# Optimization experiments

Measured on AMD Instinct MI355X. Metric: run time of the kernel, lower is better.

## Reference

```python
import jax, jax.numpy as jnp
import numpy as np

N_NODES = 50000
N_EDGES = 800000
N_REL = 8
OUT_CH = 64      # latent dim of z
HID = 128        # hidden_channels
IN_CH = 128      # reconstructed feature dim
NEG_SLOPE = 0.2


def rgat_conv(x, src, dst, edge_type, weight, q, k, bias, num_nodes):
    """PyG RGATConv, heads=1, dim=1, additive-self-attention, across-relation.
    x: [N, in]; weight: [R, in, out]; q,k: [out, 1]; bias: [out]."""
    # per-relation transform of all nodes, then per-edge gather (same math as
    # per-edge bmm with weight[edge_type], avoids [E, in, out] intermediate)
    x_all = jnp.einsum('ni,rio->nro', x, weight)          # [N, R, out]
    x_j = x_all[src, edge_type]                            # [E, out]
    x_i = x_all[dst, edge_type]                            # [E, out]
    alpha = (x_i @ q + x_j @ k)[:, 0]                      # [E]
    alpha = jax.nn.leaky_relu(alpha, NEG_SLOPE)
    # scatter-softmax over destination neighborhoods
    m = jax.ops.segment_max(alpha, dst, num_segments=num_nodes)
    m = jnp.where(jnp.isfinite(m), m, 0.0)                 # empty segments -> 0
    ex = jnp.exp(alpha - m[dst])
    denom = jax.ops.segment_sum(ex, dst, num_segments=num_nodes)
    a = ex / (denom[dst] + 1e-16)                          # [E]
    out = jax.ops.segment_sum(a[:, None] * x_j, dst, num_segments=num_nodes)
    return out + bias


def setup_inputs() -> dict:
    key = jax.random.key(0)
    ks = jax.random.split(key, 12)
    z = jax.random.normal(ks[0], (N_NODES, OUT_CH), dtype=jnp.float32)
    edge_index = jax.random.randint(ks[1], (2, N_EDGES), 0, N_NODES, dtype=jnp.int32)
    edge_type = jax.random.randint(ks[2], (N_EDGES,), 0, N_REL, dtype=jnp.int32)

    def glorot(k_, shape):
        fan = shape[-2] + shape[-1]
        return jax.random.normal(k_, shape, dtype=jnp.float32) * jnp.sqrt(2.0 / fan)

    return {
        'z': z,
        'lin_w': glorot(ks[3], (HID, OUT_CH)),
        'lin_b': jnp.zeros((HID,), dtype=jnp.float32),
        'w1': glorot(ks[4], (N_REL, HID, HID)),
        'q1': glorot(ks[5], (HID, 1)),
        'k1': glorot(ks[6], (HID, 1)),
        'b1': jnp.zeros((HID,), dtype=jnp.float32),
        'w2': glorot(ks[7], (N_REL, HID, IN_CH)),
        'q2': glorot(ks[8], (IN_CH, 1)),
        'k2': glorot(ks[9], (IN_CH, 1)),
        'b2': jnp.zeros((IN_CH,), dtype=jnp.float32),
        'edge_index': edge_index,
        'edge_type': edge_type,
    }


def reference(z, lin_w, lin_b, w1, q1, k1, b1, w2, q2, k2, b2, edge_index, edge_type):
    num_nodes = z.shape[0]
    src, dst = edge_index[0], edge_index[1]
    h = z @ lin_w.T + lin_b                                 # nn.Linear
    h = jax.nn.relu(rgat_conv(h, src, dst, edge_type, w1, q1, k1, b1, num_nodes))
    # dropout is identity in eval mode
    recon_x = rgat_conv(h, src, dst, edge_type, w2, q2, k2, b2, num_nodes)
    return recon_x
```

## Files before the change

kernel.cpp:

```cpp
#include <hip/hip_runtime.h>
#include <hip/hip_bf16.h>
#include <cstdint>
#include <cstddef>

#define N_NODES 50000
#define N_EDGES 800000
#define NSEG    (N_NODES * 8)

using frag_t = __attribute__((ext_vector_type(8))) short;
using f32x4  = __attribute__((ext_vector_type(4))) float;

typedef const __attribute__((address_space(1))) void* gptr_t;
typedef __attribute__((address_space(3))) void* lptr_t;

__device__ __forceinline__ short f2bf(float x) {
    __hip_bfloat16 h = __float2bfloat16(x);
    return *reinterpret_cast<short*>(&h);
}
__device__ __forceinline__ float bf2f(unsigned int u) {
    union { unsigned int i; float f; } v;
    v.i = u << 16;
    return v.f;
}
__device__ __forceinline__ unsigned int packbf2(float lo, float hi) {
    unsigned int a = (unsigned short)f2bf(lo);
    unsigned int b = (unsigned short)f2bf(hi);
    return a | (b << 16);
}


__global__ void hist_kernel(const int* __restrict__ dst, const int* __restrict__ et,
                            int* __restrict__ deg8, int E) {
    int e = blockIdx.x * 256 + threadIdx.x;
    if (e < E) atomicAdd(&deg8[dst[e] * 8 + et[e]], 1);
}

__global__ __launch_bounds__(256) void scan_part(const int* __restrict__ deg8,
                                                 int* __restrict__ part, int M) {
    __shared__ int red[256];
    int t = threadIdx.x;
    int idx = blockIdx.x * 1024 + t * 4;
    int s = 0;
    if (idx + 3 < M) {
        int4 d = *(const int4*)(deg8 + idx);
        s = d.x + d.y + d.z + d.w;
    } else {
        for (int c = 0; c < 4; c++) if (idx + c < M) s += deg8[idx + c];
    }
    red[t] = s;
    __syncthreads();
    #pragma unroll
    for (int off = 128; off; off >>= 1) {
        if (t < off) red[t] += red[t + off];
        __syncthreads();
    }
    if (t == 0) part[blockIdx.x] = red[0];
}

__global__ __launch_bounds__(512) void scan_mid(int* __restrict__ part, int nparts,
                                                int* __restrict__ rowp, int M) {
    __shared__ int buf[512];
    int t = threadIdx.x;
    int own = (t < nparts) ? part[t] : 0;
    buf[t] = own;
    __syncthreads();
    for (int off = 1; off < 512; off <<= 1) {
        int v = buf[t];
        int u = (t >= off) ? buf[t - off] : 0;
        __syncthreads();
        buf[t] = v + u;
        __syncthreads();
    }
    if (t < nparts) part[t] = buf[t] - own;
    if (t == 511) rowp[M] = buf[511];
}

__global__ __launch_bounds__(256) void scan_fix(const int* __restrict__ deg8,
                                                const int* __restrict__ part,
                                                int* __restrict__ rowp,
                                                int* __restrict__ cursor, int M) {
    __shared__ int wsum[4];
    int t = threadIdx.x, lane = t & 63, w = t >> 6;
    int idx = blockIdx.x * 1024 + t * 4;
    int v0 = 0, v1 = 0, v2 = 0, v3 = 0;
    if (idx + 3 < M) {
        int4 d = *(const int4*)(deg8 + idx);
        v0 = d.x; v1 = d.y; v2 = d.z; v3 = d.w;
    } else {
        if (idx     < M) v0 = deg8[idx];
        if (idx + 1 < M) v1 = deg8[idx + 1];
        if (idx + 2 < M) v2 = deg8[idx + 2];
        if (idx + 3 < M) v3 = deg8[idx + 3];
    }
    int tsum = v0 + v1 + v2 + v3;
    int sc = tsum;
    #pragma unroll
    for (int off = 1; off < 64; off <<= 1) {
        int u = __shfl_up(sc, off, 64);
        if (lane >= off) sc += u;
    }
    if (lane == 63) wsum[w] = sc;
    __syncthreads();
    int woff = 0;
    for (int i = 0; i < w; i++) woff += wsum[i];
    int excl = part[blockIdx.x] + woff + sc - tsum;
    if (idx     < M) { rowp[idx]     = excl; cursor[idx]     = excl; } excl += v0;
    if (idx + 1 < M) { rowp[idx + 1] = excl; cursor[idx + 1] = excl; } excl += v1;
    if (idx + 2 < M) { rowp[idx + 2] = excl; cursor[idx + 2] = excl; } excl += v2;
    if (idx + 3 < M) { rowp[idx + 3] = excl; cursor[idx + 3] = excl; }
}

__global__ void fill_kernel(const int* __restrict__ src, const int* __restrict__ dst,
                            const int* __restrict__ et, int* __restrict__ cursor,
                            int* __restrict__ sorted, int E) {
    int e = blockIdx.x * 256 + threadIdx.x;
    if (e < E) {
        int pos = atomicAdd(&cursor[dst[e] * 8 + et[e]], 1);
        sorted[pos] = src[e] | (et[e] << 16);
    }
}


__global__ __launch_bounds__(256) void gemm_lin(const float* __restrict__ A,
                                                const float* __restrict__ B,
                                                const float* __restrict__ bias,
                                                unsigned short* __restrict__ hb, int N) {
    const int Kdim = 64;
    __shared__ float As[32][64];
    __shared__ float Bs[32][128];
    int t = threadIdx.x;
    int n0 = blockIdx.x * 64;
    int rg = t >> 4, cg = t & 15;
    int an = t >> 2, ak = (t & 3) * 8;
    float acc[4][8] = {};

    for (int k0 = 0; k0 < Kdim; k0 += 32) {
        int gn = n0 + an;
        if (gn < N) {
            const float* ap = A + (size_t)gn * Kdim + k0 + ak;
            float4 v0 = *(const float4*)ap;
            float4 v1 = *(const float4*)(ap + 4);
            As[ak + 0][an] = v0.x; As[ak + 1][an] = v0.y;
            As[ak + 2][an] = v0.z; As[ak + 3][an] = v0.w;
            As[ak + 4][an] = v1.x; As[ak + 5][an] = v1.y;
            As[ak + 6][an] = v1.z; As[ak + 7][an] = v1.w;
        } else {
            #pragma unroll
            for (int c = 0; c < 8; c++) As[ak + c][an] = 0.f;
        }
        {
            int o = t >> 1, kh = (t & 1) * 16;
            const float* bp = B + (size_t)o * Kdim + k0 + kh;
            #pragma unroll
            for (int j = 0; j < 4; j++) {
                float4 v = ((const float4*)bp)[j];
                Bs[kh + j * 4 + 0][o] = v.x;
                Bs[kh + j * 4 + 1][o] = v.y;
                Bs[kh + j * 4 + 2][o] = v.z;
                Bs[kh + j * 4 + 3][o] = v.w;
            }
        }
        __syncthreads();
        #pragma unroll
        for (int k = 0; k < 32; k++) {
            float a[4], b[8];
            *(float4*)&a[0] = *(const float4*)&As[k][rg * 4];
            *(float4*)&b[0] = *(const float4*)&Bs[k][cg * 8];
            *(float4*)&b[4] = *(const float4*)&Bs[k][cg * 8 + 4];
            #pragma unroll
            for (int i = 0; i < 4; i++)
                #pragma unroll
                for (int j = 0; j < 8; j++)
                    acc[i][j] = fmaf(a[i], b[j], acc[i][j]);
        }
        __syncthreads();
    }
    #pragma unroll
    for (int i = 0; i < 4; i++) {
        int gn = n0 + rg * 4 + i;
        if (gn < N) {
            unsigned short us[8];
            #pragma unroll
            for (int j = 0; j < 8; j++)
                us[j] = (unsigned short)f2bf(acc[i][j] + bias[cg * 8 + j]);
            *(int4*)(hb + (size_t)gn * 128 + cg * 8) = *(int4*)&us[0];
        }
    }
}


__global__ void wprep_kernel(const float* __restrict__ W, const float* __restrict__ q,
                             const float* __restrict__ k, short* __restrict__ Bf,
                             float* __restrict__ wq, float* __restrict__ wk) {
    int g = blockIdx.x * 256 + threadIdx.x;
    if (g < 131072) {
        int kk = g >> 7, o = g & 127;
        float v = W[(size_t)kk * 128 + o];
        Bf[(((size_t)(kk >> 3) * 128) + o) * 8 + (kk & 7)] = f2bf(v);
        return;
    }
    int h = g - 131072;
    if (h < 2048) {
        int which = h >> 10;
        int r = (h >> 7) & 7;
        int i = h & 127;
        const float* vec = which ? k : q;
        const float* wrow = W + ((size_t)r * 128 + i) * 128;
        float acc = 0.f;
        #pragma unroll 4
        for (int o = 0; o < 128; o++) acc = fmaf(wrow[o], vec[o], acc);
        (which ? wk : wq)[r * 128 + i] = acc;
    }
}


__global__ __launch_bounds__(256) void qk_table_kernel(const unsigned short* __restrict__ xb,
                                                       const float* __restrict__ wq,
                                                       const float* __restrict__ wk,
                                                       float* __restrict__ Q,
                                                       float* __restrict__ K, int N) {
    int n = blockIdx.x * 256 + threadIdx.x;
    if (n >= N) return;
    const uint2* row = (const uint2*)(xb + (size_t)n * 128);
    float aq[8] = {}, ak[8] = {};
    for (int i = 0; i < 32; i++) {
        uint2 d = row[i];
        float x0 = bf2f(d.x & 0xFFFFu);
        float x1 = bf2f(d.x >> 16);
        float x2 = bf2f(d.y & 0xFFFFu);
        float x3 = bf2f(d.y >> 16);
        int c = i * 4;
        #pragma unroll
        for (int r = 0; r < 8; r++) {
            const float* wqr = wq + r * 128 + c;
            const float* wkr = wk + r * 128 + c;
            aq[r] = fmaf(x0, wqr[0], fmaf(x1, wqr[1], fmaf(x2, wqr[2], fmaf(x3, wqr[3], aq[r]))));
            ak[r] = fmaf(x0, wkr[0], fmaf(x1, wkr[1], fmaf(x2, wkr[2], fmaf(x3, wkr[3], ak[r]))));
        }
    }
    float4* qp = (float4*)(Q + (size_t)n * 8);
    qp[0] = *(float4*)&aq[0];
    qp[1] = *(float4*)&aq[4];
    float4* kp = (float4*)(K + (size_t)n * 8);
    kp[0] = *(float4*)&ak[0];
    kp[1] = *(float4*)&ak[4];
}


__global__ __launch_bounds__(512, 8) void fused_agg_gemm(
        const unsigned short* __restrict__ hb,
        const float* __restrict__ Q,
        const float* __restrict__ Kt,
        const int* __restrict__ rowp8,
        const int* __restrict__ sorted,
        const short* __restrict__ Bf,
        const float* __restrict__ bias,
        float* __restrict__ Cout,
        unsigned short* __restrict__ hbout,
        int N, int relu) {
    __shared__ short s_tile[16 * 1024];
    unsigned int* sdw = (unsigned int*)s_tile;
    const unsigned int* hbu = (const unsigned int*)hb;

    int t = threadIdx.x;
    int w = t >> 6, lane = t & 63;
    int lhi = lane >> 4, llo = lane & 15;
    int n0 = blockIdx.x * 16;

    for (int nd = 0; nd < 2; nd++) {
        int row = w * 2 + nd;
        int n = n0 + row;
        float2 acc = {0.f, 0.f};
        int rcur = 0;
        auto flushw = [&](unsigned int val) {
            int kb = rcur * 16 + (lane >> 2);
            sdw[kb * 64 + ((row ^ (kb & 15)) * 4) + (lane & 3)] = val;
        };
        if (n >= N) {
            while (rcur < 8) { flushw(0u); rcur++; }
            continue;
        }
        int beg = rowp8[n * 8];
        int end = rowp8[n * 8 + 8];
        int deg = end - beg;
        if (deg == 0) {
            while (rcur < 8) { flushw(0u); rcur++; }
            continue;
        }

        if (deg <= 64) {
            int pk = 0;
            float a = -INFINITY;
            if (lane < deg) {
                pk = sorted[beg + lane];
                int srcn = pk & 0xFFFF, etj = pk >> 16;
                a = Q[(size_t)n * 8 + etj] + Kt[(size_t)srcn * 8 + etj];
                a = (a > 0.f) ? a : 0.2f * a;
            }
            float m = a;
            #pragma unroll
            for (int off = 32; off; off >>= 1) m = fmaxf(m, __shfl_xor(m, off, 64));
            float e = (lane < deg) ? __expf(a - m) : 0.f;
            float sum = e;
            #pragma unroll
            for (int off = 32; off; off >>= 1) sum += __shfl_xor(sum, off, 64);
            float wgt = e / (sum + 1e-16f);

            int j = 0;
            for (; j + 8 <= deg; j += 8) {
                int pp[8]; float ww[8]; unsigned int dd[8];
                #pragma unroll
                for (int i = 0; i < 8; i++) {
                    pp[i] = __shfl(pk, j + i, 64);
                    ww[i] = __shfl(wgt, j + i, 64);
                }
                #pragma unroll
                for (int i = 0; i < 8; i++)
                    dd[i] = hbu[(size_t)(pp[i] & 0xFFFF) * 64 + lane];
                #pragma unroll
                for (int i = 0; i < 8; i++) {
                    int e0 = pp[i] >> 16;
                    while (rcur < e0) { flushw(packbf2(acc.x, acc.y)); acc.x = acc.y = 0.f; rcur++; }
                    acc.x = fmaf(ww[i], bf2f(dd[i] & 0xFFFF), acc.x);
                    acc.y = fmaf(ww[i], bf2f(dd[i] >> 16),    acc.y);
                }
            }
            for (; j < deg; j++) {
                int   p0 = __shfl(pk, j, 64);
                float w0 = __shfl(wgt, j, 64);
                unsigned int d0 = hbu[(size_t)(p0 & 0xFFFF) * 64 + lane];
                int e0 = p0 >> 16;
                while (rcur < e0) { flushw(packbf2(acc.x, acc.y)); acc.x = acc.y = 0.f; rcur++; }
                acc.x = fmaf(w0, bf2f(d0 & 0xFFFF), acc.x);
                acc.y = fmaf(w0, bf2f(d0 >> 16),    acc.y);
            }
            while (rcur < 8) { flushw(packbf2(acc.x, acc.y)); acc.x = acc.y = 0.f; rcur++; }
        } else {
            auto logit = [&](int j) -> float {
                int pk2 = sorted[beg + j];
                int srcn = pk2 & 0xFFFF, etj = pk2 >> 16;
                float aa = Q[(size_t)n * 8 + etj] + Kt[(size_t)srcn * 8 + etj];
                return (aa > 0.f) ? aa : 0.2f * aa;
            };
            float m = -INFINITY;
            for (int j = lane; j < deg; j += 64) m = fmaxf(m, logit(j));
            #pragma unroll
            for (int off = 32; off; off >>= 1) m = fmaxf(m, __shfl_xor(m, off, 64));
            float sum = 0.f;
            for (int j = lane; j < deg; j += 64) sum += __expf(logit(j) - m);
            #pragma unroll
            for (int off = 32; off; off >>= 1) sum += __shfl_xor(sum, off, 64);
            float inv = 1.f / (sum + 1e-16f);

            for (int j0 = 0; j0 < deg; j0 += 64) {
                int cnt = min(64, deg - j0);
                int pk = 0;
                float wgt = 0.f;
                if (lane < cnt) {
                    pk = sorted[beg + j0 + lane];
                    int srcn = pk & 0xFFFF, etj = pk >> 16;
                    float aa = Q[(size_t)n * 8 + etj] + Kt[(size_t)srcn * 8 + etj];
                    aa = (aa > 0.f) ? aa : 0.2f * aa;
                    wgt = __expf(aa - m) * inv;
                }
                for (int j = 0; j < cnt; j++) {
                    int   p0 = __shfl(pk, j, 64);
                    float w0 = __shfl(wgt, j, 64);
                    unsigned int d0 = hbu[(size_t)(p0 & 0xFFFF) * 64 + lane];
                    int e0 = p0 >> 16;
                    while (rcur < e0) { flushw(packbf2(acc.x, acc.y)); acc.x = acc.y = 0.f; rcur++; }
                    acc.x = fmaf(w0, bf2f(d0 & 0xFFFF), acc.x);
                    acc.y = fmaf(w0, bf2f(d0 >> 16),    acc.y);
                }
            }
            while (rcur < 8) { flushw(packbf2(acc.x, acc.y)); acc.x = acc.y = 0.f; rcur++; }
        }
    }
    __syncthreads();

    int ctb = w;
    f32x4 acc0 = {};
    const char* BfB = (const char*)Bf;
    #pragma unroll 4
    for (int kq = 0; kq < 32; kq++) {
        int kb = kq * 4 + lhi;
        int d = kb * 64 + ((llo ^ (kb & 15)) * 4);
        frag_t a  = *(const frag_t*)(&sdw[d]);
        frag_t b0 = *(const frag_t*)(BfB + ((size_t)kb * 128 + ctb * 16 + llo) * 16);
        acc0 = __builtin_amdgcn_mfma_f32_16x16x32_bf16(a, b0, acc0, 0, 0, 0);
    }

    {
        int col = ctb * 16 + llo;
        float bv = bias[col];
        #pragma unroll
        for (int rg = 0; rg < 4; rg++) {
            int rown = n0 + lhi * 4 + rg;
            if (rown < N) {
                float v = acc0[rg] + bv;
                if (relu) v = fmaxf(v, 0.f);
                if (Cout)  Cout[(size_t)rown * 128 + col] = v;
                if (hbout) hbout[(size_t)rown * 128 + col] = (unsigned short)f2bf(v);
            }
        }
    }
}


extern "C" void kernel_launch(void* const* d_in, const int* in_sizes, int n_in,
                              void* d_out, int out_size, void* d_ws, size_t ws_size,
                              hipStream_t stream) {
    const float* z     = (const float*)d_in[0];
    const float* lin_w = (const float*)d_in[1];
    const float* lin_b = (const float*)d_in[2];
    const float* w1    = (const float*)d_in[3];
    const float* q1    = (const float*)d_in[4];
    const float* k1    = (const float*)d_in[5];
    const float* b1    = (const float*)d_in[6];
    const float* w2    = (const float*)d_in[7];
    const float* q2    = (const float*)d_in[8];
    const float* k2    = (const float*)d_in[9];
    const float* b2    = (const float*)d_in[10];
    const int*   ei    = (const int*)d_in[11];
    const int*   et    = (const int*)d_in[12];
    float* out = (float*)d_out;

    char* ws = (char*)d_ws;
    size_t off = 0;
    auto alloc = [&](size_t bytes) -> void* {
        void* p = ws + off;
        off += (bytes + 255) & ~(size_t)255;
        return p;
    };
    unsigned short* hb  = (unsigned short*)alloc((size_t)N_NODES * 128 * 2);
    unsigned short* hb2 = (unsigned short*)alloc((size_t)N_NODES * 128 * 2);
    float* Q     = (float*)alloc((size_t)N_NODES * 8 * 4);
    float* K     = (float*)alloc((size_t)N_NODES * 8 * 4);
    int* sorted  = (int*)alloc((size_t)N_EDGES * 4);
    int* deg8    = (int*)alloc((size_t)NSEG * 4);
    int* rowp8   = (int*)alloc((size_t)(NSEG + 1) * 4);
    int* cursor8 = (int*)alloc((size_t)NSEG * 4);
    int* part    = (int*)alloc(1024 * 4);
    float* wq    = (float*)alloc(8 * 128 * 4);
    float* wk    = (float*)alloc(8 * 128 * 4);
    short* Bf    = (short*)alloc((size_t)1024 * 128 * 2);

    const int* src = ei;
    const int* dst = ei + N_EDGES;

    const int M = NSEG;
    const int nparts = (M + 1023) / 1024;

    hipMemsetAsync(deg8, 0, (size_t)M * 4, stream);
    hist_kernel<<<(N_EDGES + 255) / 256, 256, 0, stream>>>(dst, et, deg8, N_EDGES);
    scan_part<<<nparts, 256, 0, stream>>>(deg8, part, M);
    scan_mid<<<1, 512, 0, stream>>>(part, nparts, rowp8, M);
    scan_fix<<<nparts, 256, 0, stream>>>(deg8, part, rowp8, cursor8, M);
    fill_kernel<<<(N_EDGES + 255) / 256, 256, 0, stream>>>(src, dst, et, cursor8, sorted, N_EDGES);

    gemm_lin<<<(N_NODES + 63) / 64, 256, 0, stream>>>(z, lin_w, lin_b, hb, N_NODES);

    int fgrid = (N_NODES + 15) / 16;
    int qgrid = (N_NODES + 255) / 256;
    int wgrid = (131072 + 2048) / 256;

    wprep_kernel<<<wgrid, 256, 0, stream>>>(w1, q1, k1, Bf, wq, wk);
    qk_table_kernel<<<qgrid, 256, 0, stream>>>(hb, wq, wk, Q, K, N_NODES);
    fused_agg_gemm<<<fgrid, 512, 0, stream>>>(hb, Q, K, rowp8, sorted, Bf, b1,
                                              (float*)nullptr, hb2, N_NODES, 1);

    wprep_kernel<<<wgrid, 256, 0, stream>>>(w2, q2, k2, Bf, wq, wk);
    qk_table_kernel<<<qgrid, 256, 0, stream>>>(hb2, wq, wk, Q, K, N_NODES);
    fused_agg_gemm<<<fgrid, 512, 0, stream>>>(hb2, Q, K, rowp8, sorted, Bf, b2,
                                              out, (unsigned short*)nullptr, N_NODES, 0);
}
```

Baseline: 375.1 us.

## Process nodes in descending-degree order via counting-sort permutation in fused aggregation

Builds a permutation of nodes sorted by in-degree (descending, capped at 255) using a histogram, a single-block scan and an atomic fill. The fused aggregate+GEMM kernel then processes nodes in that order, so each 16-node tile holds nodes of similar degree and heavy tiles start first. It writes outputs through the permuted node ids. The aim is less load imbalance and wave divergence inside blocks, at the cost of extra setup kernels and scattered output rows and inputs.

Result: slower. 626.3 us (+67.0%).

```diff
diff --git a/kernel.cpp b/kernel.cpp
--- a/kernel.cpp
+++ b/kernel.cpp
@@ -112,11 +112,42 @@
 
 __global__ void fill_kernel(const int* __restrict__ src, const int* __restrict__ dst,
                             const int* __restrict__ et, int* __restrict__ cursor,
-                            int* __restrict__ sorted, int E) {
+                            int* __restrict__ sorted, int E,
+                            const int* __restrict__ rowp8, int* __restrict__ dcount, int N) {
     int e = blockIdx.x * 256 + threadIdx.x;
     if (e < E) {
         int pos = atomicAdd(&cursor[dst[e] * 8 + et[e]], 1);
         sorted[pos] = src[e] | (et[e] << 16);
+    }
+    if (e < N) {
+        int d = min(rowp8[e * 8 + 8] - rowp8[e * 8], 255);
+        atomicAdd(&dcount[255 - d], 1);
+    }
+}
+
+__global__ __launch_bounds__(256) void deg_scan_kernel(const int* __restrict__ dcount,
+                                                       int* __restrict__ dcursor) {
+    __shared__ int buf[256];
+    int t = threadIdx.x;
+    int v = dcount[t];
+    buf[t] = v;
+    __syncthreads();
+    for (int off = 1; off < 256; off <<= 1) {
+        int u = (t >= off) ? buf[t - off] : 0;
+        __syncthreads();
+        buf[t] += u;
+        __syncthreads();
+    }
+    dcursor[t] = buf[t] - v;
+}
+
+__global__ void deg_fill_kernel(const int* __restrict__ rowp8, int* __restrict__ dcursor,
+                                int* __restrict__ perm, int N) {
+    int n = blockIdx.x * 256 + threadIdx.x;
+    if (n < N) {
+        int d = min(rowp8[n * 8 + 8] - rowp8[n * 8], 255);
+        int pos = atomicAdd(&dcursor[255 - d], 1);
+        perm[pos] = n;
     }
 }
 
@@ -253,12 +284,14 @@
         const float* __restrict__ Kt,
         const int* __restrict__ rowp8,
         const int* __restrict__ sorted,
+        const int* __restrict__ perm,
         const short* __restrict__ Bf,
         const float* __restrict__ bias,
         float* __restrict__ Cout,
         unsigned short* __restrict__ hbout,
         int N, int relu) {
     __shared__ short s_tile[16 * 1024];
+    __shared__ int nid_tile[16];
     unsigned int* sdw = (unsigned int*)s_tile;
     const unsigned int* hbu = (const unsigned int*)hb;
 
@@ -269,14 +302,16 @@
 
     for (int nd = 0; nd < 2; nd++) {
         int row = w * 2 + nd;
-        int n = n0 + row;
+        int vrow = n0 + row;
+        int n = (vrow < N) ? perm[vrow] : -1;
+        if (lane == 0) nid_tile[row] = n;
         float2 acc = {0.f, 0.f};
         int rcur = 0;
         auto flushw = [&](unsigned int val) {
             int kb = rcur * 16 + (lane >> 2);
             sdw[kb * 64 + ((row ^ (kb & 15)) * 4) + (lane & 3)] = val;
         };
-        if (n >= N) {
+        if (n < 0) {
             while (rcur < 8) { flushw(0u); rcur++; }
             continue;
         }
@@ -395,12 +430,12 @@
         float bv = bias[col];
         #pragma unroll
         for (int rg = 0; rg < 4; rg++) {
-            int rown = n0 + lhi * 4 + rg;
-            if (rown < N) {
+            int nid = nid_tile[lhi * 4 + rg];
+            if (nid >= 0) {
                 float v = acc0[rg] + bv;
                 if (relu) v = fmaxf(v, 0.f);
-                if (Cout)  Cout[(size_t)rown * 128 + col] = v;
-                if (hbout) hbout[(size_t)rown * 128 + col] = (unsigned short)f2bf(v);
+                if (Cout)  Cout[(size_t)nid * 128 + col] = v;
+                if (hbout) hbout[(size_t)nid * 128 + col] = (unsigned short)f2bf(v);
             }
         }
     }
@@ -441,6 +476,9 @@
     int* rowp8   = (int*)alloc((size_t)(NSEG + 1) * 4);
     int* cursor8 = (int*)alloc((size_t)NSEG * 4);
     int* part    = (int*)alloc(1024 * 4);
+    int* perm    = (int*)alloc((size_t)N_NODES * 4);
+    int* dcount  = (int*)alloc(256 * 4);
+    int* dcursor = (int*)alloc(256 * 4);
     float* wq    = (float*)alloc(8 * 128 * 4);
     float* wk    = (float*)alloc(8 * 128 * 4);
     short* Bf    = (short*)alloc((size_t)1024 * 128 * 2);
@@ -452,11 +490,15 @@
     const int nparts = (M + 1023) / 1024;
 
     hipMemsetAsync(deg8, 0, (size_t)M * 4, stream);
+    hipMemsetAsync(dcount, 0, 256 * 4, stream);
     hist_kernel<<<(N_EDGES + 255) / 256, 256, 0, stream>>>(dst, et, deg8, N_EDGES);
     scan_part<<<nparts, 256, 0, stream>>>(deg8, part, M);
     scan_mid<<<1, 512, 0, stream>>>(part, nparts, rowp8, M);
     scan_fix<<<nparts, 256, 0, stream>>>(deg8, part, rowp8, cursor8, M);
-    fill_kernel<<<(N_EDGES + 255) / 256, 256, 0, stream>>>(src, dst, et, cursor8, sorted, N_EDGES);
+    fill_kernel<<<(N_EDGES + 255) / 256, 256, 0, stream>>>(src, dst, et, cursor8, sorted,
+                                                           N_EDGES, rowp8, dcount, N_NODES);
+    deg_scan_kernel<<<1, 256, 0, stream>>>(dcount, dcursor);
+    deg_fill_kernel<<<(N_NODES + 255) / 256, 256, 0, stream>>>(rowp8, dcursor, perm, N_NODES);
 
     gemm_lin<<<(N_NODES + 63) / 64, 256, 0, stream>>>(z, lin_w, lin_b, hb, N_NODES);
 
@@ -466,11 +508,11 @@
 
     wprep_kernel<<<wgrid, 256, 0, stream>>>(w1, q1, k1, Bf, wq, wk);
     qk_table_kernel<<<qgrid, 256, 0, stream>>>(hb, wq, wk, Q, K, N_NODES);
-    fused_agg_gemm<<<fgrid, 512, 0, stream>>>(hb, Q, K, rowp8, sorted, Bf, b1,
+    fused_agg_gemm<<<fgrid, 512, 0, stream>>>(hb, Q, K, rowp8, sorted, perm, Bf, b1,
                                               (float*)nullptr, hb2, N_NODES, 1);
 
     wprep_kernel<<<wgrid, 256, 0, stream>>>(w2, q2, k2, Bf, wq, wk);
     qk_table_kernel<<<qgrid, 256, 0, stream>>>(hb2, wq, wk, Q, K, N_NODES);
-    fused_agg_gemm<<<fgrid, 512, 0, stream>>>(hb2, Q, K, rowp8, sorted, Bf, b2,
+    fused_agg_gemm<<<fgrid, 512, 0, stream>>>(hb2, Q, K, rowp8, sorted, perm, Bf, b2,
                                               out, (unsigned short*)nullptr, N_NODES, 0);
 }
```

## Dynamically assign rows to waves and broadcast edge data via LDS stash

Applied to the files above, without the earlier changes.

Replaces the fixed two-rows-per-wave assignment with an LDS atomic counter, so waves pull destination rows dynamically and degree imbalance is evened out within a block. Per-edge packed index and softmax weight are stored once into a per-wave LDS stash and read back as broadcast loads, instead of two cross-lane shuffles per edge. This adds an atomic per row, an extra barrier and some extra LDS usage, which may reduce occupancy slightly.

After: 377.1 us. Within noise of the previous version (+0.5%).

```diff
diff --git a/kernel.cpp b/kernel.cpp
--- a/kernel.cpp
+++ b/kernel.cpp
@@ -259,6 +259,8 @@
         unsigned short* __restrict__ hbout,
         int N, int relu) {
     __shared__ short s_tile[16 * 1024];
+    __shared__ uint2 stash[8][64];
+    __shared__ int wcnt;
     unsigned int* sdw = (unsigned int*)s_tile;
     const unsigned int* hbu = (const unsigned int*)hb;
 
@@ -267,8 +269,14 @@
     int lhi = lane >> 4, llo = lane & 15;
     int n0 = blockIdx.x * 16;
 
-    for (int nd = 0; nd < 2; nd++) {
-        int row = w * 2 + nd;
+    if (t == 0) wcnt = 0;
+    __syncthreads();
+
+    for (;;) {
+        int row;
+        if (lane == 0) row = atomicAdd(&wcnt, 1);
+        row = __shfl(row, 0, 64);
+        if (row >= 16) break;
         int n = n0 + row;
         float2 acc = {0.f, 0.f};
         int rcur = 0;
@@ -305,31 +313,30 @@
             #pragma unroll
             for (int off = 32; off; off >>= 1) sum += __shfl_xor(sum, off, 64);
             float wgt = e / (sum + 1e-16f);
+            stash[w][lane] = make_uint2((unsigned int)pk, __float_as_uint(wgt));
 
             int j = 0;
             for (; j + 8 <= deg; j += 8) {
-                int pp[8]; float ww[8]; unsigned int dd[8];
+                uint2 ee[8]; unsigned int dd[8];
+                #pragma unroll
+                for (int i = 0; i < 8; i++) ee[i] = stash[w][j + i];
+                #pragma unroll
+                for (int i = 0; i < 8; i++)
+                    dd[i] = hbu[(size_t)(ee[i].x & 0xFFFFu) * 64 + lane];
                 #pragma unroll
                 for (int i = 0; i < 8; i++) {
-                    pp[i] = __shfl(pk, j + i, 64);
-                    ww[i] = __shfl(wgt, j + i, 64);
+                    int e0 = (int)(ee[i].x >> 16);
+                    float w0 = __uint_as_float(ee[i].y);
+                    while (rcur < e0) { flushw(packbf2(acc.x, acc.y)); acc.x = acc.y = 0.f; rcur++; }
+                    acc.x = fmaf(w0, bf2f(dd[i] & 0xFFFF), acc.x);
+                    acc.y = fmaf(w0, bf2f(dd[i] >> 16),    acc.y);
                 }
-                #pragma unroll
-                for (int i = 0; i < 8; i++)
-                    dd[i] = hbu[(size_t)(pp[i] & 0xFFFF) * 64 + lane];
-                #pragma unroll
-                for (int i = 0; i < 8; i++) {
-                    int e0 = pp[i] >> 16;
-                    while (rcur < e0) { flushw(packbf2(acc.x, acc.y)); acc.x = acc.y = 0.f; rcur++; }
-                    acc.x = fmaf(ww[i], bf2f(dd[i] & 0xFFFF), acc.x);
-                    acc.y = fmaf(ww[i], bf2f(dd[i] >> 16),    acc.y);
-                }
             }
             for (; j < deg; j++) {
-                int   p0 = __shfl(pk, j, 64);
-                float w0 = __shfl(wgt, j, 64);
-                unsigned int d0 = hbu[(size_t)(p0 & 0xFFFF) * 64 + lane];
-                int e0 = p0 >> 16;
+                uint2 e1 = stash[w][j];
+                unsigned int d0 = hbu[(size_t)(e1.x & 0xFFFFu) * 64 + lane];
+                int e0 = (int)(e1.x >> 16);
+                float w0 = __uint_as_float(e1.y);
                 while (rcur < e0) { flushw(packbf2(acc.x, acc.y)); acc.x = acc.y = 0.f; rcur++; }
                 acc.x = fmaf(w0, bf2f(d0 & 0xFFFF), acc.x);
                 acc.y = fmaf(w0, bf2f(d0 >> 16),    acc.y);
@@ -354,20 +361,19 @@
 
             for (int j0 = 0; j0 < deg; j0 += 64) {
                 int cnt = min(64, deg - j0);
-                int pk = 0;
-                float wgt = 0.f;
                 if (lane < cnt) {
-                    pk = sorted[beg + j0 + lane];
+                    int pk = sorted[beg + j0 + lane];
                     int srcn = pk & 0xFFFF, etj = pk >> 16;
                     float aa = Q[(size_t)n * 8 + etj] + Kt[(size_t)srcn * 8 + etj];
                     aa = (aa > 0.f) ? aa : 0.2f * aa;
-                    wgt = __expf(aa - m) * inv;
+                    float wgt = __expf(aa - m) * inv;
+                    stash[w][lane] = make_uint2((unsigned int)pk, __float_as_uint(wgt));
                 }
                 for (int j = 0; j < cnt; j++) {
-                    int   p0 = __shfl(pk, j, 64);
-                    float w0 = __shfl(wgt, j, 64);
-                    unsigned int d0 = hbu[(size_t)(p0 & 0xFFFF) * 64 + lane];
-                    int e0 = p0 >> 16;
+                    uint2 e1 = stash[w][j];
+                    unsigned int d0 = hbu[(size_t)(e1.x & 0xFFFFu) * 64 + lane];
+                    int e0 = (int)(e1.x >> 16);
+                    float w0 = __uint_as_float(e1.y);
                     while (rcur < e0) { flushw(packbf2(acc.x, acc.y)); acc.x = acc.y = 0.f; rcur++; }
                     acc.x = fmaf(w0, bf2f(d0 & 0xFFFF), acc.x);
                     acc.y = fmaf(w0, bf2f(d0 >> 16),    acc.y);
```
